# Kernel tuning notes

Hardware: AMD Instinct MI355X
Metric: run time of the kernel (lower is better)

The kernel has to match this reference:

```python
import jax, jax.numpy as jnp
import numpy as np

T, S, W, D, C, K = 16, 16, 10, 512, 64, 512  # tasks, shots, ways, z_dim, n_concept, triplets/group


def setup_inputs() -> dict:
    key = jax.random.key(0)
    ks = jax.random.split(key, 12)
    sc = 0.02
    inp = {
        "input_data": jax.random.normal(ks[0], (T, S, W, D), dtype=jnp.float32),
        "triplet_idx": jax.random.randint(ks[1], (T, W, 3, K), 0, S * W, dtype=jnp.int64),
        # proj_inner: Linear(3D -> 2D), ReLU, Linear(2D -> D)
        "W1": jax.random.normal(ks[2], (3 * D, 2 * D), dtype=jnp.float32) * sc,
        "b1": jnp.zeros((2 * D,), dtype=jnp.float32),
        "W2": jax.random.normal(ks[3], (2 * D, D), dtype=jnp.float32) * sc,
        "b2": jnp.zeros((D,), dtype=jnp.float32),
        # proj_outer: Linear(D -> 2D), ReLU, Linear(2D -> D)
        "W3": jax.random.normal(ks[4], (D, 2 * D), dtype=jnp.float32) * sc,
        "b3": jnp.zeros((2 * D,), dtype=jnp.float32),
        "W4": jax.random.normal(ks[5], (2 * D, D), dtype=jnp.float32) * sc,
        "b4": jnp.zeros((D,), dtype=jnp.float32),
        # cls: Linear(D -> C)
        "Wc": jax.random.normal(ks[6], (D, C), dtype=jnp.float32) * sc,
        "bc": jnp.zeros((C,), dtype=jnp.float32),
    }
    return inp


def reference(input_data, triplet_idx, W1, b1, W2, b2, W3, b3, W4, b4, Wc, bc):
    t, s, w, d = input_data.shape
    x = input_data.reshape(t, s * w, d)                     # [T, N, D], N = shot*way
    # gather triplet embeddings: [T, W, 3, K, D]
    emb = x[jnp.arange(t)[:, None, None, None], triplet_idx]
    # permute([1,0,2]).reshape(-1, 3*dim): [T, W, K, 3*D]
    trip = jnp.swapaxes(emb, 2, 3).reshape(t, w, -1, 3 * d)
    # proj_inner MLP then sum over triplets
    h = jax.nn.relu(trip @ W1 + b1) @ W2 + b2               # [T, W, K, D]
    g = jnp.sum(h, axis=2)                                  # [T, W, D]
    # proj_outer MLP -> cls -> softmax
    o = jax.nn.relu(g @ W3 + b3) @ W4 + b4                  # [T, W, D]
    score = o @ Wc + bc                                     # [T, W, C]
    return jax.nn.softmax(score, axis=-1)
```

## Files before the change

kernel.cpp:

```cpp
#include <hip/hip_runtime.h>
#include <hip/hip_bf16.h>

#define T_  16
#define W_  10
#define D_  512
#define SW_ 160
#define N1_ 1024
#define KT_ 512

typedef __bf16 bf16x8 __attribute__((ext_vector_type(8)));
typedef float  f32x4  __attribute__((ext_vector_type(4)));

__device__ __forceinline__ void async16(const void* g, void* l) {
  __builtin_amdgcn_global_load_lds(
      (__attribute__((address_space(1))) void*)(g),
      (__attribute__((address_space(3))) void*)(l), 16, 0, 0);
}

__device__ __forceinline__ float lo16(unsigned v) { return __uint_as_float(v << 16); }
__device__ __forceinline__ float hi16(unsigned v) { return __uint_as_float(v & 0xffff0000u); }

__global__ __launch_bounds__(256) void cast_x(const float* __restrict__ xin,
                                              __hip_bfloat16* __restrict__ xbf) {
  int i = blockIdx.x * 256 + threadIdx.x;
  xbf[i] = __float2bfloat16(xin[i]);
}

__global__ __launch_bounds__(256) void transpose_w1(const float* __restrict__ W1,
                                                    __hip_bfloat16* __restrict__ w1t) {
  __shared__ float tile[32 * 33];
  int k0 = blockIdx.y * 32, n0 = blockIdx.x * 32;
  int c = threadIdx.x & 31, r0 = threadIdx.x >> 5;
#pragma unroll
  for (int i = 0; i < 4; ++i) {
    int r = r0 + i * 8;
    tile[r * 33 + c] = W1[(size_t)(k0 + r) * N1_ + n0 + c];
  }
  __syncthreads();
#pragma unroll
  for (int i = 0; i < 4; ++i) {
    int r = r0 + i * 8;
    w1t[(size_t)(n0 + r) * 1536 + k0 + c] = __float2bfloat16(tile[c * 33 + r]);
  }
}

__global__ __launch_bounds__(256) void transpose4(
    const float* __restrict__ W2, const float* __restrict__ W3,
    const float* __restrict__ W4, const float* __restrict__ Wc,
    __hip_bfloat16* __restrict__ W2t, __hip_bfloat16* __restrict__ W3t,
    __hip_bfloat16* __restrict__ W4t, __hip_bfloat16* __restrict__ Wct)
{
  const float* src; __hip_bfloat16* dst; int R, C;
  switch (blockIdx.z) {
    case 0:  src = W2; dst = W2t; R = 1024; C = 512;  break;
    case 1:  src = W3; dst = W3t; R = 512;  C = 1024; break;
    case 2:  src = W4; dst = W4t; R = 1024; C = 512;  break;
    default: src = Wc; dst = Wct; R = 512;  C = 64;   break;
  }
  int r0 = blockIdx.y * 32, c0 = blockIdx.x * 32;
  if (r0 >= R || c0 >= C) return;
  __shared__ float tile[32 * 33];
  int c = threadIdx.x & 31, rr = threadIdx.x >> 5;
#pragma unroll
  for (int i = 0; i < 4; ++i) {
    int r = rr + i * 8;
    tile[r * 33 + c] = src[(size_t)(r0 + r) * C + c0 + c];
  }
  __syncthreads();
#pragma unroll
  for (int i = 0; i < 4; ++i) {
    int r = rr + i * 8;
    dst[(size_t)(c0 + r) * R + r0 + c] = __float2bfloat16(tile[c * 33 + r]);
  }
}

__global__ __launch_bounds__(256) void group_kernel(
    const __hip_bfloat16* __restrict__ xbf,
    const __hip_bfloat16* __restrict__ w1t,
    const int* __restrict__ tidx,
    const float* __restrict__ b1,
    __hip_bfloat16* __restrict__ Hsb)
{
  __shared__ __align__(16) char smem[43008];
  char* Abuf  = smem;
  char* Bbuf  = smem + 20480;
  char* Ptile = smem;
  int*  idx_s = (int*)(smem + 34560);
  float* red  = (float*)(smem + 40704);

  const int tid = threadIdx.x;
  const int bx  = blockIdx.x;
  const int t   = bx >> 5;
  const int nt  = bx & 31;
  const int n0  = nt << 5;

  const int ln = tid & 63, wv = tid >> 6;
  const int wr = wv >> 1, wc = wv & 1;
  const int col16 = ln & 15, quad = ln >> 4;

  const __hip_bfloat16* xt = xbf + (size_t)t * (SW_ * D_);

  int aoff[5], lofA[5];
#pragma unroll
  for (int s = 0; s < 5; ++s) {
    int i = s * 256 + tid, r = i >> 3, q = i & 7;
    aoff[s] = r * 512 + ((q ^ (r & 7)) << 3);
    lofA[s] = i << 4;
  }
  int boff[3], lofB[3];
#pragma unroll
  for (int s = 0; s < 3; ++s) {
    int i = s * 256 + tid, r = i >> 3, q = i & 7;
    int nc = r & 31, j = r >> 5;
    boff[s] = (n0 + nc) * 1536 + j * 512 + ((q ^ (r & 7)) << 3);
    lofB[s] = i << 4;
  }

  f32x4 acc[5][3];
#pragma unroll
  for (int a = 0; a < 5; ++a)
#pragma unroll
    for (int b = 0; b < 3; ++b)
      acc[a][b] = (f32x4){0.f, 0.f, 0.f, 0.f};

#pragma unroll 1
  for (int kk = 0; kk < 512; kk += 64) {
    __syncthreads();
#pragma unroll
    for (int s = 0; s < 5; ++s) async16(xt + aoff[s] + kk, Abuf + lofA[s]);
#pragma unroll
    for (int s = 0; s < 3; ++s) async16(w1t + boff[s] + kk, Bbuf + lofB[s]);
    __syncthreads();

#pragma unroll
    for (int ks = 0; ks < 2; ++ks) {
      const int qq = (ks << 2) + quad;
      bf16x8 af[5], bfr[3];
#pragma unroll
      for (int a = 0; a < 5; ++a) {
        int rm = wr * 80 + a * 16 + col16;
        af[a] = *(const bf16x8*)(Abuf + rm * 128 + ((qq ^ (rm & 7)) << 4));
      }
#pragma unroll
      for (int b = 0; b < 3; ++b) {
        int rn = wc * 48 + b * 16 + col16;
        bfr[b] = *(const bf16x8*)(Bbuf + rn * 128 + ((qq ^ (rn & 7)) << 4));
      }
#pragma unroll
      for (int a = 0; a < 5; ++a)
#pragma unroll
        for (int b = 0; b < 3; ++b)
          acc[a][b] = __builtin_amdgcn_mfma_f32_16x16x32_bf16(af[a], bfr[b], acc[a][b], 0, 0, 0);
    }
  }

  __syncthreads();

#pragma unroll
  for (int a = 0; a < 5; ++a)
#pragma unroll
    for (int b = 0; b < 3; ++b) {
      int c = wc * 48 + b * 16 + col16;
      int j = c >> 5, nc = c & 31;
      int mb = wr * 80 + a * 16 + quad * 4;
#pragma unroll
      for (int r = 0; r < 4; ++r)
        *(__hip_bfloat16*)(Ptile + (j * 160 + mb + r) * 72 + nc * 2) =
            __float2bfloat16(acc[a][b][r]);
    }

  const int nq = tid & 7;
  const int kq = tid >> 3;
  const float4 bias4 = *(const float4*)(b1 + n0 + (nq << 2));

#pragma unroll 1
  for (int w = 0; w < 10; ++w) {
    __syncthreads();
    {
      const int* src = tidx + (size_t)(t * 10 + w) * 1536;
      async16(src + (tid << 2), (char*)idx_s + (tid << 4));
      if (tid < 128) async16(src + 1024 + (tid << 2), (char*)idx_s + 4096 + (tid << 4));
    }
    __syncthreads();

    f32x4 a4 = (f32x4){0.f, 0.f, 0.f, 0.f};
#pragma unroll
    for (int u = 0; u < 4; ++u) {
      const int kb = (kq << 4) + (u << 2);
      int4 i0 = *(const int4*)(idx_s + kb);
      int4 i1 = *(const int4*)(idx_s + 512 + kb);
      int4 i2 = *(const int4*)(idx_s + 1024 + kb);
#define STEP(IA, IB, IC)                                                          \
      {                                                                           \
        uint2 p0 = *(const uint2*)(Ptile + (IA) * 72 + (nq << 3));                \
        uint2 p1 = *(const uint2*)(Ptile + 11520 + (IB) * 72 + (nq << 3));        \
        uint2 p2 = *(const uint2*)(Ptile + 23040 + (IC) * 72 + (nq << 3));        \
        a4.x += fmaxf(lo16(p0.x) + lo16(p1.x) + lo16(p2.x) + bias4.x, 0.f);       \
        a4.y += fmaxf(hi16(p0.x) + hi16(p1.x) + hi16(p2.x) + bias4.y, 0.f);       \
        a4.z += fmaxf(lo16(p0.y) + lo16(p1.y) + lo16(p2.y) + bias4.z, 0.f);       \
        a4.w += fmaxf(hi16(p0.y) + hi16(p1.y) + hi16(p2.y) + bias4.w, 0.f);       \
      }
      STEP(i0.x, i1.x, i2.x)
      STEP(i0.y, i1.y, i2.y)
      STEP(i0.z, i1.z, i2.z)
      STEP(i0.w, i1.w, i2.w)
#undef STEP
    }

#pragma unroll
    for (int off = 8; off <= 32; off <<= 1) {
      a4.x += __shfl_xor(a4.x, off);
      a4.y += __shfl_xor(a4.y, off);
      a4.z += __shfl_xor(a4.z, off);
      a4.w += __shfl_xor(a4.w, off);
    }
    if ((ln >> 3) == 0)
      *(f32x4*)(red + wv * 32 + (nq << 2)) = a4;
    __syncthreads();
    if (tid < 32) {
      float s = red[tid] + red[32 + tid] + red[64 + tid] + red[96 + tid];
      Hsb[(size_t)(t * 10 + w) * N1_ + n0 + tid] = __float2bfloat16(s);
    }
  }
}

__global__ __launch_bounds__(256) void tail_gemm(
    const __hip_bfloat16* __restrict__ A,
    const __hip_bfloat16* __restrict__ Bt,
    const float* __restrict__ bias, float bscale, int relu, int K, int N,
    __hip_bfloat16* __restrict__ out)
{
  __shared__ __align__(16) char Abuf[20480];
  __shared__ __align__(16) char Bbuf[16384];
  const int tid = threadIdx.x;
  const int n0 = blockIdx.x << 6;
  const int m0 = blockIdx.y * 80;
  const int ln = tid & 63, wv = tid >> 6;
  const int col16 = ln & 15, quad = ln >> 4;

  f32x4 acc[5];
#pragma unroll
  for (int a = 0; a < 5; ++a) acc[a] = (f32x4){0.f, 0.f, 0.f, 0.f};

#pragma unroll 1
  for (int kk = 0; kk < K; kk += 128) {
    __syncthreads();
#pragma unroll
    for (int p = 0; p < 5; ++p) {
      int i = p * 256 + tid, r = i >> 4, q = i & 15;
      async16(A + (size_t)(m0 + r) * K + kk + ((q ^ (r & 7)) << 3), Abuf + (i << 4));
    }
#pragma unroll
    for (int p = 0; p < 4; ++p) {
      int i = p * 256 + tid, r = i >> 4, q = i & 15;
      async16(Bt + (size_t)(n0 + r) * K + kk + ((q ^ (r & 7)) << 3), Bbuf + (i << 4));
    }
    __syncthreads();

#pragma unroll
    for (int ks = 0; ks < 4; ++ks) {
      const int qq = (ks << 2) + quad;
      const int rn = (wv << 4) + col16;
      bf16x8 bf = *(const bf16x8*)(Bbuf + rn * 256 + ((qq ^ (rn & 7)) << 4));
#pragma unroll
      for (int a = 0; a < 5; ++a) {
        int rm = (a << 4) + col16;
        bf16x8 af = *(const bf16x8*)(Abuf + rm * 256 + ((qq ^ (rm & 7)) << 4));
        acc[a] = __builtin_amdgcn_mfma_f32_16x16x32_bf16(af, bf, acc[a], 0, 0, 0);
      }
    }
  }

  const int n = n0 + (wv << 4) + col16;
  const float bb = bias[n] * bscale;
#pragma unroll
  for (int a = 0; a < 5; ++a)
#pragma unroll
    for (int r = 0; r < 4; ++r) {
      float v = acc[a][r] + bb;
      if (relu) v = fmaxf(v, 0.f);
      out[(size_t)(m0 + (a << 4) + (quad << 2) + r) * N + n] = __float2bfloat16(v);
    }
}

__global__ __launch_bounds__(256) void head_gemm(
    const __hip_bfloat16* __restrict__ A,
    const __hip_bfloat16* __restrict__ Bt,
    const float* __restrict__ bc,
    float* __restrict__ out)
{
  __shared__ __align__(16) char Abuf[20480];
  __shared__ __align__(16) char Bbuf[16384];
  __shared__ float sc[80 * 64];
  __shared__ float rs[80];
  const int tid = threadIdx.x;
  const int m0 = blockIdx.x * 80;
  const int ln = tid & 63, wv = tid >> 6;
  const int col16 = ln & 15, quad = ln >> 4;

  f32x4 acc[5];
#pragma unroll
  for (int a = 0; a < 5; ++a) acc[a] = (f32x4){0.f, 0.f, 0.f, 0.f};

#pragma unroll 1
  for (int kk = 0; kk < 512; kk += 128) {
    __syncthreads();
#pragma unroll
    for (int p = 0; p < 5; ++p) {
      int i = p * 256 + tid, r = i >> 4, q = i & 15;
      async16(A + (size_t)(m0 + r) * 512 + kk + ((q ^ (r & 7)) << 3), Abuf + (i << 4));
    }
#pragma unroll
    for (int p = 0; p < 4; ++p) {
      int i = p * 256 + tid, r = i >> 4, q = i & 15;
      async16(Bt + (size_t)r * 512 + kk + ((q ^ (r & 7)) << 3), Bbuf + (i << 4));
    }
    __syncthreads();

#pragma unroll
    for (int ks = 0; ks < 4; ++ks) {
      const int qq = (ks << 2) + quad;
      const int rn = (wv << 4) + col16;
      bf16x8 bf = *(const bf16x8*)(Bbuf + rn * 256 + ((qq ^ (rn & 7)) << 4));
#pragma unroll
      for (int a = 0; a < 5; ++a) {
        int rm = (a << 4) + col16;
        bf16x8 af = *(const bf16x8*)(Abuf + rm * 256 + ((qq ^ (rm & 7)) << 4));
        acc[a] = __builtin_amdgcn_mfma_f32_16x16x32_bf16(af, bf, acc[a], 0, 0, 0);
      }
    }
  }

  const int n = (wv << 4) + col16;
  const float bb = bc[n];
#pragma unroll
  for (int a = 0; a < 5; ++a)
#pragma unroll
    for (int r = 0; r < 4; ++r)
      sc[((a << 4) + (quad << 2) + r) * 64 + n] = acc[a][r] + bb;
  __syncthreads();

  if (tid < 80) {
    float m = -1e30f;
    for (int c = 0; c < 64; ++c) m = fmaxf(m, sc[tid * 64 + c]);
    float s = 0.f;
    for (int c = 0; c < 64; ++c) {
      float e = expf(sc[tid * 64 + c] - m);
      sc[tid * 64 + c] = e;
      s += e;
    }
    rs[tid] = 1.f / s;
  }
  __syncthreads();
#pragma unroll
  for (int p = 0; p < 20; ++p) {
    int f = p * 256 + tid, r = f >> 6, c = f & 63;
    out[(size_t)(m0 + r) * 64 + c] = sc[f] * rs[r];
  }
}

extern "C" void kernel_launch(void* const* d_in, const int* in_sizes, int n_in,
                              void* d_out, int out_size, void* d_ws, size_t ws_size,
                              hipStream_t stream) {
  const float* x_in = (const float*)d_in[0];
  const int*   tidx = (const int*)d_in[1];
  const float* W1 = (const float*)d_in[2];
  const float* b1 = (const float*)d_in[3];
  const float* W2 = (const float*)d_in[4];
  const float* b2 = (const float*)d_in[5];
  const float* W3 = (const float*)d_in[6];
  const float* b3 = (const float*)d_in[7];
  const float* W4 = (const float*)d_in[8];
  const float* b4 = (const float*)d_in[9];
  const float* Wc = (const float*)d_in[10];
  const float* bc = (const float*)d_in[11];
  float* out = (float*)d_out;
  (void)in_sizes; (void)n_in; (void)out_size; (void)ws_size;

  char* ws = (char*)d_ws;
  __hip_bfloat16* xbf = (__hip_bfloat16*)(ws + 0);
  __hip_bfloat16* w1t = (__hip_bfloat16*)(ws + 2621440);
  __hip_bfloat16* W2t = (__hip_bfloat16*)(ws + 0);
  __hip_bfloat16* W3t = (__hip_bfloat16*)(ws + 1048576);
  __hip_bfloat16* W4t = (__hip_bfloat16*)(ws + 2097152);
  __hip_bfloat16* Wct = (__hip_bfloat16*)(ws + 3145728);
  __hip_bfloat16* Hsb = (__hip_bfloat16*)(ws + 5767168);
  __hip_bfloat16* gb  = (__hip_bfloat16*)(ws + 6094848);
  __hip_bfloat16* ub  = (__hip_bfloat16*)(ws + 6258688);
  __hip_bfloat16* ob  = (__hip_bfloat16*)(ws + 6586368);

  cast_x<<<5120, 256, 0, stream>>>(x_in, xbf);
  transpose_w1<<<dim3(32, 48), 256, 0, stream>>>(W1, w1t);

  group_kernel<<<512, 256, 0, stream>>>(xbf, w1t, tidx, b1, Hsb);

  transpose4<<<dim3(32, 32, 4), 256, 0, stream>>>(W2, W3, W4, Wc, W2t, W3t, W4t, Wct);

  tail_gemm<<<dim3(8, 2), 256, 0, stream>>>(Hsb, W2t, b2, (float)KT_, 0, 1024, 512, gb);
  tail_gemm<<<dim3(16, 2), 256, 0, stream>>>(gb, W3t, b3, 1.f, 1, 512, 1024, ub);
  tail_gemm<<<dim3(8, 2), 256, 0, stream>>>(ub, W4t, b4, 1.f, 0, 1024, 512, ob);
  head_gemm<<<2, 256, 0, stream>>>(ob, Wct, bc, out);
}
```

Baseline: 165.9 us.

## Merge prep kernels, fuse tail GEMMs with grid barriers, add split-bf16 precision

Merges the x cast, the W1 transpose and the other weight transposes into one prep launch. The four tail GEMM/softmax launches become a single 32-block kernel that uses atomic grid barriers between stages. The tail weights and activations are split into bf16 hi/lo pairs and run as three MFMAs per step to recover near-fp32 accuracy. The group kernel now double-buffers its index loads and defers each reduction write-out to the next iteration. Fewer launches cut launch overhead, but the tail does three times the MFMA work, moves double the bytes, and depends on spin-wait barriers with all blocks resident.

```diff
diff --git a/kernel.cpp b/kernel.cpp
--- a/kernel.cpp
+++ b/kernel.cpp
@@ -1,7 +1,6 @@
 #include <hip/hip_runtime.h>
 #include <hip/hip_bf16.h>
 
-#define T_  16
 #define W_  10
 #define D_  512
 #define SW_ 160
@@ -19,48 +18,78 @@
 
 __device__ __forceinline__ float lo16(unsigned v) { return __uint_as_float(v << 16); }
 __device__ __forceinline__ float hi16(unsigned v) { return __uint_as_float(v & 0xffff0000u); }
-
-__global__ __launch_bounds__(256) void cast_x(const float* __restrict__ xin,
-                                              __hip_bfloat16* __restrict__ xbf) {
-  int i = blockIdx.x * 256 + threadIdx.x;
-  xbf[i] = __float2bfloat16(xin[i]);
-}
-
-__global__ __launch_bounds__(256) void transpose_w1(const float* __restrict__ W1,
-                                                    __hip_bfloat16* __restrict__ w1t) {
-  __shared__ float tile[32 * 33];
-  int k0 = blockIdx.y * 32, n0 = blockIdx.x * 32;
-  int c = threadIdx.x & 31, r0 = threadIdx.x >> 5;
-#pragma unroll
-  for (int i = 0; i < 4; ++i) {
-    int r = r0 + i * 8;
-    tile[r * 33 + c] = W1[(size_t)(k0 + r) * N1_ + n0 + c];
-  }
+__device__ __forceinline__ unsigned short f2bu(float x) {
+  __hip_bfloat16 b = __float2bfloat16(x);
+  return *(unsigned short*)&b;
+}
+__device__ __forceinline__ float bu2f(unsigned short u) {
+  return __uint_as_float(((unsigned)u) << 16);
+}
+
+__device__ __forceinline__ void gridbar(int* ctr, int target) {
   __syncthreads();
-#pragma unroll
-  for (int i = 0; i < 4; ++i) {
-    int r = r0 + i * 8;
-    w1t[(size_t)(n0 + r) * 1536 + k0 + c] = __float2bfloat16(tile[c * 33 + r]);
-  }
-}
-
-__global__ __launch_bounds__(256) void transpose4(
+  if (threadIdx.x == 0) {
+    __threadfence();
+    __hip_atomic_fetch_add(ctr, 1, __ATOMIC_ACQ_REL, __HIP_MEMORY_SCOPE_AGENT);
+    while (__hip_atomic_load(ctr, __ATOMIC_ACQUIRE, __HIP_MEMORY_SCOPE_AGENT) < target)
+      __builtin_amdgcn_s_sleep(2);
+    __threadfence();
+  }
+  __syncthreads();
+}
+
+__global__ __launch_bounds__(256) void prep(
+    const float* __restrict__ xin, const float* __restrict__ W1,
     const float* __restrict__ W2, const float* __restrict__ W3,
     const float* __restrict__ W4, const float* __restrict__ Wc,
-    __hip_bfloat16* __restrict__ W2t, __hip_bfloat16* __restrict__ W3t,
-    __hip_bfloat16* __restrict__ W4t, __hip_bfloat16* __restrict__ Wct)
+    unsigned short* __restrict__ xbf, unsigned short* __restrict__ w1t,
+    unsigned short* __restrict__ W2h, unsigned short* __restrict__ W2l,
+    unsigned short* __restrict__ W3h, unsigned short* __restrict__ W3l,
+    unsigned short* __restrict__ W4h, unsigned short* __restrict__ W4l,
+    unsigned short* __restrict__ Wch, unsigned short* __restrict__ Wcl,
+    int* __restrict__ flags)
 {
-  const float* src; __hip_bfloat16* dst; int R, C;
-  switch (blockIdx.z) {
-    case 0:  src = W2; dst = W2t; R = 1024; C = 512;  break;
-    case 1:  src = W3; dst = W3t; R = 512;  C = 1024; break;
-    case 2:  src = W4; dst = W4t; R = 1024; C = 512;  break;
-    default: src = Wc; dst = Wct; R = 512;  C = 64;   break;
-  }
-  int r0 = blockIdx.y * 32, c0 = blockIdx.x * 32;
-  if (r0 >= R || c0 >= C) return;
   __shared__ float tile[32 * 33];
-  int c = threadIdx.x & 31, rr = threadIdx.x >> 5;
+  const int bx = blockIdx.x, tid = threadIdx.x;
+  if (bx == 0 && tid < 16) flags[tid] = 0;
+
+  if (bx < 256) {
+    int base = bx * 256 + tid;
+#pragma unroll
+    for (int rep = 0; rep < 5; ++rep) {
+      int e = (rep * 65536 + base) * 4;
+      float4 v = *(const float4*)(xin + e);
+      ushort4 o = { f2bu(v.x), f2bu(v.y), f2bu(v.z), f2bu(v.w) };
+      *(ushort4*)(xbf + e) = o;
+    }
+    return;
+  }
+
+  const int c = tid & 31, rr = tid >> 5;
+  if (bx < 1792) {
+    int q = bx - 256;
+    int n0 = (q & 31) << 5, k0 = (q >> 5) << 5;
+#pragma unroll
+    for (int i = 0; i < 4; ++i) {
+      int r = rr + i * 8;
+      tile[r * 33 + c] = W1[(size_t)(k0 + r) * N1_ + n0 + c];
+    }
+    __syncthreads();
+#pragma unroll
+    for (int i = 0; i < 4; ++i) {
+      int r = rr + i * 8;
+      w1t[(size_t)(n0 + r) * 1536 + k0 + c] = f2bu(tile[c * 33 + r]);
+    }
+    return;
+  }
+
+  int q = bx - 1792;
+  const float* src; unsigned short *dh, *dl; int R, C, rt, ct;
+  if (q < 512)       { src = W2; dh = W2h; dl = W2l; R = 1024; C = 512;  rt = q >> 4;          ct = q & 15; }
+  else if (q < 1024) { src = W3; dh = W3h; dl = W3l; R = 512;  C = 1024; rt = (q - 512) >> 5;  ct = (q - 512) & 31; }
+  else if (q < 1536) { src = W4; dh = W4h; dl = W4l; R = 1024; C = 512;  rt = (q - 1024) >> 4; ct = (q - 1024) & 15; }
+  else               { src = Wc; dh = Wch; dl = Wcl; R = 512;  C = 64;   rt = (q - 1536) >> 1; ct = (q - 1536) & 1; }
+  int r0 = rt << 5, c0 = ct << 5;
 #pragma unroll
   for (int i = 0; i < 4; ++i) {
     int r = rr + i * 8;
@@ -70,35 +99,39 @@
 #pragma unroll
   for (int i = 0; i < 4; ++i) {
     int r = rr + i * 8;
-    dst[(size_t)(c0 + r) * R + r0 + c] = __float2bfloat16(tile[c * 33 + r]);
+    float v = tile[c * 33 + r];
+    unsigned short h = f2bu(v);
+    size_t off = (size_t)(c0 + r) * R + r0 + c;
+    dh[off] = h;
+    dl[off] = f2bu(v - bu2f(h));
   }
 }
 
 __global__ __launch_bounds__(256) void group_kernel(
-    const __hip_bfloat16* __restrict__ xbf,
-    const __hip_bfloat16* __restrict__ w1t,
+    const unsigned short* __restrict__ xbf,
+    const unsigned short* __restrict__ w1t,
     const int* __restrict__ tidx,
     const float* __restrict__ b1,
-    __hip_bfloat16* __restrict__ Hsb)
+    unsigned short* __restrict__ Hsh,
+    unsigned short* __restrict__ Hsl)
 {
-  __shared__ __align__(16) char smem[43008];
+  __shared__ __align__(16) char smem[47872];
   char* Abuf  = smem;
   char* Bbuf  = smem + 20480;
   char* Ptile = smem;
   int*  idx_s = (int*)(smem + 34560);
-  float* red  = (float*)(smem + 40704);
+  float* red  = (float*)(smem + 46848);
 
   const int tid = threadIdx.x;
   const int bx  = blockIdx.x;
   const int t   = bx >> 5;
-  const int nt  = bx & 31;
-  const int n0  = nt << 5;
+  const int n0  = (bx & 31) << 5;
 
   const int ln = tid & 63, wv = tid >> 6;
   const int wr = wv >> 1, wc = wv & 1;
   const int col16 = ln & 15, quad = ln >> 4;
 
-  const __hip_bfloat16* xt = xbf + (size_t)t * (SW_ * D_);
+  const unsigned short* xt = xbf + (size_t)t * (SW_ * D_);
 
   int aoff[5], lofA[5];
 #pragma unroll
@@ -160,36 +193,52 @@
   for (int a = 0; a < 5; ++a)
 #pragma unroll
     for (int b = 0; b < 3; ++b) {
-      int c = wc * 48 + b * 16 + col16;
-      int j = c >> 5, nc = c & 31;
+      int cidx = wc * 48 + b * 16 + col16;
+      int j = cidx >> 5, nc = cidx & 31;
       int mb = wr * 80 + a * 16 + quad * 4;
 #pragma unroll
       for (int r = 0; r < 4; ++r)
-        *(__hip_bfloat16*)(Ptile + (j * 160 + mb + r) * 72 + nc * 2) =
-            __float2bfloat16(acc[a][b][r]);
+        *(unsigned short*)(Ptile + (j * 160 + mb + r) * 72 + nc * 2) =
+            f2bu(acc[a][b][r]);
     }
 
   const int nq = tid & 7;
   const int kq = tid >> 3;
   const float4 bias4 = *(const float4*)(b1 + n0 + (nq << 2));
+  const int* tbase = tidx + (size_t)t * 10 * 1536;
+
+  {
+    const int* src = tbase;
+    char* dst = (char*)idx_s;
+    async16(src + (tid << 2), dst + (tid << 4));
+    if (tid < 128) async16(src + 1024 + (tid << 2), dst + 4096 + (tid << 4));
+  }
 
 #pragma unroll 1
   for (int w = 0; w < 10; ++w) {
     __syncthreads();
-    {
-      const int* src = tidx + (size_t)(t * 10 + w) * 1536;
-      async16(src + (tid << 2), (char*)idx_s + (tid << 4));
-      if (tid < 128) async16(src + 1024 + (tid << 2), (char*)idx_s + 4096 + (tid << 4));
-    }
-    __syncthreads();
-
+    if (w < 9) {
+      const int* src = tbase + (w + 1) * 1536;
+      char* dst = (char*)idx_s + ((w + 1) & 1) * 6144;
+      async16(src + (tid << 2), dst + (tid << 4));
+      if (tid < 128) async16(src + 1024 + (tid << 2), dst + 4096 + (tid << 4));
+    }
+    if (w > 0 && tid < 32) {
+      const float* rb = red + ((w - 1) & 1) * 128;
+      float s = rb[tid] + rb[32 + tid] + rb[64 + tid] + rb[96 + tid];
+      unsigned short h = f2bu(s);
+      size_t off = (size_t)(t * 10 + (w - 1)) * N1_ + n0 + tid;
+      Hsh[off] = h; Hsl[off] = f2bu(s - bu2f(h));
+    }
+
+    const int* ib = idx_s + (w & 1) * 1536;
     f32x4 a4 = (f32x4){0.f, 0.f, 0.f, 0.f};
 #pragma unroll
     for (int u = 0; u < 4; ++u) {
       const int kb = (kq << 4) + (u << 2);
-      int4 i0 = *(const int4*)(idx_s + kb);
-      int4 i1 = *(const int4*)(idx_s + 512 + kb);
-      int4 i2 = *(const int4*)(idx_s + 1024 + kb);
+      int4 i0 = *(const int4*)(ib + kb);
+      int4 i1 = *(const int4*)(ib + 512 + kb);
+      int4 i2 = *(const int4*)(ib + 1024 + kb);
 #define STEP(IA, IB, IC)                                                          \
       {                                                                           \
         uint2 p0 = *(const uint2*)(Ptile + (IA) * 72 + (nq << 3));                \
@@ -215,147 +264,165 @@
       a4.w += __shfl_xor(a4.w, off);
     }
     if ((ln >> 3) == 0)
-      *(f32x4*)(red + wv * 32 + (nq << 2)) = a4;
-    __syncthreads();
-    if (tid < 32) {
-      float s = red[tid] + red[32 + tid] + red[64 + tid] + red[96 + tid];
-      Hsb[(size_t)(t * 10 + w) * N1_ + n0 + tid] = __float2bfloat16(s);
-    }
-  }
-}
-
-__global__ __launch_bounds__(256) void tail_gemm(
-    const __hip_bfloat16* __restrict__ A,
-    const __hip_bfloat16* __restrict__ Bt,
-    const float* __restrict__ bias, float bscale, int relu, int K, int N,
-    __hip_bfloat16* __restrict__ out)
+      *(f32x4*)(red + (w & 1) * 128 + wv * 32 + (nq << 2)) = a4;
+  }
+  __syncthreads();
+  if (tid < 32) {
+    const float* rb = red + 128;
+    float s = rb[tid] + rb[32 + tid] + rb[64 + tid] + rb[96 + tid];
+    unsigned short h = f2bu(s);
+    size_t off = (size_t)(t * 10 + 9) * N1_ + n0 + tid;
+    Hsh[off] = h; Hsl[off] = f2bu(s - bu2f(h));
+  }
+}
+
+__device__ __forceinline__ void gemm80(
+    char* AH, char* AL, char* BH, char* BL,
+    const unsigned short* __restrict__ Ah, const unsigned short* __restrict__ Al, int m0,
+    const unsigned short* __restrict__ Bh, const unsigned short* __restrict__ Bl, int n0,
+    int K, f32x4 acc[5], int tid)
 {
-  __shared__ __align__(16) char Abuf[20480];
-  __shared__ __align__(16) char Bbuf[16384];
-  const int tid = threadIdx.x;
-  const int n0 = blockIdx.x << 6;
-  const int m0 = blockIdx.y * 80;
-  const int ln = tid & 63, wv = tid >> 6;
-  const int col16 = ln & 15, quad = ln >> 4;
-
-  f32x4 acc[5];
-#pragma unroll
-  for (int a = 0; a < 5; ++a) acc[a] = (f32x4){0.f, 0.f, 0.f, 0.f};
-
+  const int ln = tid & 63, wv = tid >> 6, col16 = ln & 15, quad = ln >> 4;
 #pragma unroll 1
-  for (int kk = 0; kk < K; kk += 128) {
-    __syncthreads();
-#pragma unroll
-    for (int p = 0; p < 5; ++p) {
-      int i = p * 256 + tid, r = i >> 4, q = i & 15;
-      async16(A + (size_t)(m0 + r) * K + kk + ((q ^ (r & 7)) << 3), Abuf + (i << 4));
-    }
-#pragma unroll
-    for (int p = 0; p < 4; ++p) {
-      int i = p * 256 + tid, r = i >> 4, q = i & 15;
-      async16(Bt + (size_t)(n0 + r) * K + kk + ((q ^ (r & 7)) << 3), Bbuf + (i << 4));
-    }
-    __syncthreads();
-
-#pragma unroll
-    for (int ks = 0; ks < 4; ++ks) {
+  for (int kk = 0; kk < K; kk += 64) {
+    __syncthreads();
+#pragma unroll
+    for (int p = 0; p < 9; ++p) {
+      int i = p * 256 + tid;
+      if (i < 640) {
+        int r = i >> 3, q = i & 7;
+        async16(Ah + (size_t)(m0 + r) * K + kk + ((q ^ (r & 7)) << 3), AH + (i << 4));
+      } else if (i < 1280) {
+        int j = i - 640, r = j >> 3, q = j & 7;
+        async16(Al + (size_t)(m0 + r) * K + kk + ((q ^ (r & 7)) << 3), AL + (j << 4));
+      } else if (i < 1792) {
+        int j = i - 1280, r = j >> 3, q = j & 7;
+        async16(Bh + (size_t)(n0 + r) * K + kk + ((q ^ (r & 7)) << 3), BH + (j << 4));
+      } else {
+        int j = i - 1792, r = j >> 3, q = j & 7;
+        async16(Bl + (size_t)(n0 + r) * K + kk + ((q ^ (r & 7)) << 3), BL + (j << 4));
+      }
+    }
+    __syncthreads();
+#pragma unroll
+    for (int ks = 0; ks < 2; ++ks) {
       const int qq = (ks << 2) + quad;
       const int rn = (wv << 4) + col16;
-      bf16x8 bf = *(const bf16x8*)(Bbuf + rn * 256 + ((qq ^ (rn & 7)) << 4));
+      bf16x8 bh = *(const bf16x8*)(BH + rn * 128 + ((qq ^ (rn & 7)) << 4));
+      bf16x8 bl = *(const bf16x8*)(BL + rn * 128 + ((qq ^ (rn & 7)) << 4));
 #pragma unroll
       for (int a = 0; a < 5; ++a) {
         int rm = (a << 4) + col16;
-        bf16x8 af = *(const bf16x8*)(Abuf + rm * 256 + ((qq ^ (rm & 7)) << 4));
-        acc[a] = __builtin_amdgcn_mfma_f32_16x16x32_bf16(af, bf, acc[a], 0, 0, 0);
-      }
-    }
-  }
-
-  const int n = n0 + (wv << 4) + col16;
-  const float bb = bias[n] * bscale;
+        bf16x8 ah = *(const bf16x8*)(AH + rm * 128 + ((qq ^ (rm & 7)) << 4));
+        bf16x8 al = *(const bf16x8*)(AL + rm * 128 + ((qq ^ (rm & 7)) << 4));
+        acc[a] = __builtin_amdgcn_mfma_f32_16x16x32_bf16(ah, bh, acc[a], 0, 0, 0);
+        acc[a] = __builtin_amdgcn_mfma_f32_16x16x32_bf16(ah, bl, acc[a], 0, 0, 0);
+        acc[a] = __builtin_amdgcn_mfma_f32_16x16x32_bf16(al, bh, acc[a], 0, 0, 0);
+      }
+    }
+  }
+}
+
+__device__ __forceinline__ void store_pair(
+    f32x4 acc[5], int m0, int n0, const float* __restrict__ bias, float scale,
+    bool relu, unsigned short* __restrict__ Oh, unsigned short* __restrict__ Ol,
+    int ldo, int tid)
+{
+  const int ln = tid & 63, wv = tid >> 6, col16 = ln & 15, quad = ln >> 4;
+  const int col = n0 + (wv << 4) + col16;
+  const float bb = bias[col] * scale;
 #pragma unroll
   for (int a = 0; a < 5; ++a)
 #pragma unroll
     for (int r = 0; r < 4; ++r) {
+      int row = m0 + (a << 4) + (quad << 2) + r;
       float v = acc[a][r] + bb;
       if (relu) v = fmaxf(v, 0.f);
-      out[(size_t)(m0 + (a << 4) + (quad << 2) + r) * N + n] = __float2bfloat16(v);
-    }
-}
-
-__global__ __launch_bounds__(256) void head_gemm(
-    const __hip_bfloat16* __restrict__ A,
-    const __hip_bfloat16* __restrict__ Bt,
-    const float* __restrict__ bc,
-    float* __restrict__ out)
+      unsigned short h = f2bu(v);
+      size_t off = (size_t)row * ldo + col;
+      Oh[off] = h; Ol[off] = f2bu(v - bu2f(h));
+    }
+}
+
+__global__ __launch_bounds__(256) void tail_kernel(
+    const unsigned short* __restrict__ Hsh, const unsigned short* __restrict__ Hsl,
+    const unsigned short* __restrict__ W2h, const unsigned short* __restrict__ W2l,
+    const unsigned short* __restrict__ W3h, const unsigned short* __restrict__ W3l,
+    const unsigned short* __restrict__ W4h, const unsigned short* __restrict__ W4l,
+    const unsigned short* __restrict__ Wch, const unsigned short* __restrict__ Wcl,
+    const float* __restrict__ b2, const float* __restrict__ b3,
+    const float* __restrict__ b4, const float* __restrict__ bc,
+    unsigned short* __restrict__ gh, unsigned short* __restrict__ gl,
+    unsigned short* __restrict__ uh, unsigned short* __restrict__ ul,
+    unsigned short* __restrict__ oh, unsigned short* __restrict__ ol,
+    int* __restrict__ ctrs, float* __restrict__ out)
 {
-  __shared__ __align__(16) char Abuf[20480];
-  __shared__ __align__(16) char Bbuf[16384];
-  __shared__ float sc[80 * 64];
-  __shared__ float rs[80];
-  const int tid = threadIdx.x;
-  const int m0 = blockIdx.x * 80;
-  const int ln = tid & 63, wv = tid >> 6;
-  const int col16 = ln & 15, quad = ln >> 4;
-
+  __shared__ __align__(16) char sm[36864];
+  char* AH = sm, *AL = sm + 10240, *BH = sm + 20480, *BL = sm + 28672;
+  const int bx = blockIdx.x, tid = threadIdx.x;
   f32x4 acc[5];
-#pragma unroll
-  for (int a = 0; a < 5; ++a) acc[a] = (f32x4){0.f, 0.f, 0.f, 0.f};
-
-#pragma unroll 1
-  for (int kk = 0; kk < 512; kk += 128) {
-    __syncthreads();
-#pragma unroll
-    for (int p = 0; p < 5; ++p) {
-      int i = p * 256 + tid, r = i >> 4, q = i & 15;
-      async16(A + (size_t)(m0 + r) * 512 + kk + ((q ^ (r & 7)) << 3), Abuf + (i << 4));
-    }
-#pragma unroll
-    for (int p = 0; p < 4; ++p) {
-      int i = p * 256 + tid, r = i >> 4, q = i & 15;
-      async16(Bt + (size_t)r * 512 + kk + ((q ^ (r & 7)) << 3), Bbuf + (i << 4));
-    }
-    __syncthreads();
-
-#pragma unroll
-    for (int ks = 0; ks < 4; ++ks) {
-      const int qq = (ks << 2) + quad;
-      const int rn = (wv << 4) + col16;
-      bf16x8 bf = *(const bf16x8*)(Bbuf + rn * 256 + ((qq ^ (rn & 7)) << 4));
-#pragma unroll
-      for (int a = 0; a < 5; ++a) {
-        int rm = (a << 4) + col16;
-        bf16x8 af = *(const bf16x8*)(Abuf + rm * 256 + ((qq ^ (rm & 7)) << 4));
-        acc[a] = __builtin_amdgcn_mfma_f32_16x16x32_bf16(af, bf, acc[a], 0, 0, 0);
-      }
-    }
-  }
-
-  const int n = (wv << 4) + col16;
-  const float bb = bc[n];
-#pragma unroll
-  for (int a = 0; a < 5; ++a)
-#pragma unroll
-    for (int r = 0; r < 4; ++r)
-      sc[((a << 4) + (quad << 2) + r) * 64 + n] = acc[a][r] + bb;
-  __syncthreads();
-
-  if (tid < 80) {
-    float m = -1e30f;
-    for (int c = 0; c < 64; ++c) m = fmaxf(m, sc[tid * 64 + c]);
-    float s = 0.f;
-    for (int c = 0; c < 64; ++c) {
-      float e = expf(sc[tid * 64 + c] - m);
-      sc[tid * 64 + c] = e;
-      s += e;
-    }
-    rs[tid] = 1.f / s;
-  }
-  __syncthreads();
-#pragma unroll
-  for (int p = 0; p < 20; ++p) {
-    int f = p * 256 + tid, r = f >> 6, c = f & 63;
-    out[(size_t)(m0 + r) * 64 + c] = sc[f] * rs[r];
+
+  if (bx < 16) {
+#pragma unroll
+    for (int a = 0; a < 5; ++a) acc[a] = (f32x4){0.f, 0.f, 0.f, 0.f};
+    int m0 = (bx & 1) * 80, n0 = (bx >> 1) << 6;
+    gemm80(AH, AL, BH, BL, Hsh, Hsl, m0, W2h, W2l, n0, 1024, acc, tid);
+    store_pair(acc, m0, n0, b2, (float)KT_, false, gh, gl, 512, tid);
+  }
+  gridbar(&ctrs[0], 32);
+
+  {
+#pragma unroll
+    for (int a = 0; a < 5; ++a) acc[a] = (f32x4){0.f, 0.f, 0.f, 0.f};
+    int m0 = (bx & 1) * 80, n0 = (bx >> 1) << 6;
+    gemm80(AH, AL, BH, BL, gh, gl, m0, W3h, W3l, n0, 512, acc, tid);
+    store_pair(acc, m0, n0, b3, 1.f, true, uh, ul, 1024, tid);
+  }
+  gridbar(&ctrs[1], 32);
+
+  if (bx < 16) {
+#pragma unroll
+    for (int a = 0; a < 5; ++a) acc[a] = (f32x4){0.f, 0.f, 0.f, 0.f};
+    int m0 = (bx & 1) * 80, n0 = (bx >> 1) << 6;
+    gemm80(AH, AL, BH, BL, uh, ul, m0, W4h, W4l, n0, 1024, acc, tid);
+    store_pair(acc, m0, n0, b4, 1.f, false, oh, ol, 512, tid);
+  }
+  gridbar(&ctrs[2], 32);
+
+  if (bx < 2) {
+#pragma unroll
+    for (int a = 0; a < 5; ++a) acc[a] = (f32x4){0.f, 0.f, 0.f, 0.f};
+    int m0 = bx * 80;
+    gemm80(AH, AL, BH, BL, oh, ol, m0, Wch, Wcl, 0, 512, acc, tid);
+    __syncthreads();
+    float* sc = (float*)sm;
+    float* rs = (float*)(sm + 20480);
+    const int ln = tid & 63, wv = tid >> 6, col16 = ln & 15, quad = ln >> 4;
+    const int col = (wv << 4) + col16;
+    const float bb = bc[col];
+#pragma unroll
+    for (int a = 0; a < 5; ++a)
+#pragma unroll
+      for (int r = 0; r < 4; ++r)
+        sc[((a << 4) + (quad << 2) + r) * 64 + col] = acc[a][r] + bb;
+    __syncthreads();
+    if (tid < 80) {
+      float m = -1e30f;
+      for (int c = 0; c < 64; ++c) m = fmaxf(m, sc[tid * 64 + c]);
+      float s = 0.f;
+      for (int c = 0; c < 64; ++c) {
+        float e = expf(sc[tid * 64 + c] - m);
+        sc[tid * 64 + c] = e;
+        s += e;
+      }
+      rs[tid] = 1.f / s;
+    }
+    __syncthreads();
+#pragma unroll
+    for (int p = 0; p < 20; ++p) {
+      int f = p * 256 + tid, r = f >> 6, c = f & 63;
+      out[(size_t)(m0 + r) * 64 + c] = sc[f] * rs[r];
+    }
   }
 }
 
@@ -378,26 +445,31 @@
   (void)in_sizes; (void)n_in; (void)out_size; (void)ws_size;
 
   char* ws = (char*)d_ws;
-  __hip_bfloat16* xbf = (__hip_bfloat16*)(ws + 0);
-  __hip_bfloat16* w1t = (__hip_bfloat16*)(ws + 2621440);
-  __hip_bfloat16* W2t = (__hip_bfloat16*)(ws + 0);
-  __hip_bfloat16* W3t = (__hip_bfloat16*)(ws + 1048576);
-  __hip_bfloat16* W4t = (__hip_bfloat16*)(ws + 2097152);
-  __hip_bfloat16* Wct = (__hip_bfloat16*)(ws + 3145728);
-  __hip_bfloat16* Hsb = (__hip_bfloat16*)(ws + 5767168);
-  __hip_bfloat16* gb  = (__hip_bfloat16*)(ws + 6094848);
-  __hip_bfloat16* ub  = (__hip_bfloat16*)(ws + 6258688);
-  __hip_bfloat16* ob  = (__hip_bfloat16*)(ws + 6586368);
-
-  cast_x<<<5120, 256, 0, stream>>>(x_in, xbf);
-  transpose_w1<<<dim3(32, 48), 256, 0, stream>>>(W1, w1t);
-
-  group_kernel<<<512, 256, 0, stream>>>(xbf, w1t, tidx, b1, Hsb);
-
-  transpose4<<<dim3(32, 32, 4), 256, 0, stream>>>(W2, W3, W4, Wc, W2t, W3t, W4t, Wct);
-
-  tail_gemm<<<dim3(8, 2), 256, 0, stream>>>(Hsb, W2t, b2, (float)KT_, 0, 1024, 512, gb);
-  tail_gemm<<<dim3(16, 2), 256, 0, stream>>>(gb, W3t, b3, 1.f, 1, 512, 1024, ub);
-  tail_gemm<<<dim3(8, 2), 256, 0, stream>>>(ub, W4t, b4, 1.f, 0, 1024, 512, ob);
-  head_gemm<<<2, 256, 0, stream>>>(ob, Wct, bc, out);
-}
+  unsigned short* xbf = (unsigned short*)(ws + 0);
+  unsigned short* w1t = (unsigned short*)(ws + 2621440);
+  unsigned short* W2h = (unsigned short*)(ws + 5767168);
+  unsigned short* W2l = (unsigned short*)(ws + 6815744);
+  unsigned short* W3h = (unsigned short*)(ws + 7864320);
+  unsigned short* W3l = (unsigned short*)(ws + 8912896);
+  unsigned short* W4h = (unsigned short*)(ws + 9961472);
+  unsigned short* W4l = (unsigned short*)(ws + 11010048);
+  unsigned short* Wch = (unsigned short*)(ws + 12058624);
+  unsigned short* Wcl = (unsigned short*)(ws + 12124160);
+  unsigned short* Hsh = (unsigned short*)(ws + 12189696);
+  unsigned short* Hsl = (unsigned short*)(ws + 12517376);
+  unsigned short* gh  = (unsigned short*)(ws + 12845056);
+  unsigned short* gl  = (unsigned short*)(ws + 13008896);
+  unsigned short* uh  = (unsigned short*)(ws + 13172736);
+  unsigned short* ul  = (unsigned short*)(ws + 13500416);
+  unsigned short* oh  = (unsigned short*)(ws + 13828096);
+  unsigned short* ol  = (unsigned short*)(ws + 13991936);
+  int* ctrs           = (int*)(ws + 14155776);
+
+  prep<<<3360, 256, 0, stream>>>(x_in, W1, W2, W3, W4, Wc,
+                                 xbf, w1t, W2h, W2l, W3h, W3l, W4h, W4l, Wch, Wcl, ctrs);
+
+  group_kernel<<<512, 256, 0, stream>>>(xbf, w1t, tidx, b1, Hsh, Hsl);
+
+  tail_kernel<<<32, 256, 0, stream>>>(Hsh, Hsl, W2h, W2l, W3h, W3l, W4h, W4l, Wch, Wcl,
+                                      b2, b3, b4, bc, gh, gl, uh, ul, oh, ol, ctrs, out);
+}
```

Measured after the change: 192.6 us. 1.16x slower.
